# Optimization experiments

Hardware: AMD Instinct MI355X
Metric: run time of the kernel (lower is better)

## Reference

```python
import jax, jax.numpy as jnp
import numpy as np

B, C, N = 4, 256, 4096
OUT = 256
TEMP = OUT ** 0.5  # temperature = sqrt(out_channel)


def setup_inputs() -> dict:
    key = jax.random.key(0)
    kx, kxx, kq, kk, kv = jax.random.split(key, 5)
    x = jax.random.normal(kx, (B, C, N), dtype=jnp.float32)
    xx = jax.random.normal(kxx, (B, C, N), dtype=jnp.float32)
    # Conv1d(in, out, kernel=1, bias=False) weights, squeezed to (out, in)
    s = 1.0 / np.sqrt(C)
    Wq = jax.random.uniform(kq, (OUT, C), jnp.float32, -s, s)
    Wk = jax.random.uniform(kk, (OUT, C), jnp.float32, -s, s)
    Wv = jax.random.uniform(kv, (OUT, C), jnp.float32, -s, s)
    return {"x": x, "xx": xx, "Wq": Wq, "Wk": Wk, "Wv": Wv}


def reference(x, xx, Wq, Wk, Wv):
    # 1x1 conv == per-point linear: (out,in) x (b,in,n) -> (b,out,n)
    q = jnp.einsum('oc,bcn->bon', Wq, x)
    k = jnp.einsum('oc,bcn->bon', Wk, xx)
    v = jnp.einsum('oc,bcn->bon', Wv, xx)
    # attn = (q^T / temp) @ k : (B, N, N)
    attn = jax.nn.softmax(jnp.einsum('bon,bom->bnm', q, k) / TEMP, axis=-1)
    # dropout is identity in eval mode
    # y = attn @ v^T -> (B, N, OUT); returned transposed to (B, OUT, N)
    y = jnp.einsum('bnm,bom->bon', attn, v)
    return y
```

## Files before the change

kernel.cpp:

```cpp
#include <hip/hip_runtime.h>
#include <hip/hip_bf16.h>


typedef __attribute__((ext_vector_type(8))) short bf16x8;
typedef __attribute__((ext_vector_type(4))) float f32x4;
typedef __attribute__((ext_vector_type(4))) short short4t;

constexpr int B_ = 4;
constexpr int C_ = 256;
constexpr int N_ = 4096;
constexpr int O_ = 256;
constexpr float INV_TEMP = 1.0f / 16.0f;
constexpr int NIT = 64;

__device__ __forceinline__ short f2bf(float f) {
  union { float f; unsigned u; } v; v.f = f;
  unsigned r = v.u + 0x7fffu + ((v.u >> 16) & 1u);
  return (short)(r >> 16);
}

__global__ void wcvt(const float* __restrict__ Wq, const float* __restrict__ Wk,
                     const float* __restrict__ Wv, short* __restrict__ wb) {
  int i = blockIdx.x * 256 + threadIdx.x;
  int mat = i >> 16, off = i & 65535;
  const float* W = (mat == 0) ? Wq : (mat == 1 ? Wk : Wv);
  wb[i] = f2bf(W[off]);
}

__global__ __launch_bounds__(256, 2) void qkv_proj(
    const float* __restrict__ x, const float* __restrict__ xx,
    const short* __restrict__ wb,
    short* __restrict__ qg, short* __restrict__ kt, short* __restrict__ vt) {
  const int n0  = blockIdx.x * 64;
  const int b   = blockIdx.y;
  const int mat = blockIdx.z;
  const float* src = (mat == 0) ? x : xx;
  const short* W   = wb + mat * 65536;
  const int tid = threadIdx.x;
  const int w = tid >> 6, lane = tid & 63;
  const int g = lane >> 4, c16 = lane & 15;

  __shared__ __align__(16) short xs[64][264];

  {
    const int n = tid & 63, cq = tid >> 6;
    const float* sp = src + (size_t)b * C_ * N_ + n0 + n;
    float xr[64];
#pragma unroll
    for (int rep = 0; rep < 16; ++rep)
#pragma unroll
      for (int j = 0; j < 4; ++j)
        xr[rep * 4 + j] = sp[(size_t)(rep * 16 + cq * 4 + j) * N_];
#pragma unroll
    for (int rep = 0; rep < 16; ++rep) {
      int c = rep * 16 + cq * 4;
      short4t s4;
#pragma unroll
      for (int j = 0; j < 4; ++j) s4[j] = f2bf(xr[rep * 4 + j]);
      *(short4t*)&xs[n][c] = s4;
    }
  }
  __syncthreads();

  f32x4 acc[4][4];
#pragma unroll
  for (int i = 0; i < 4; ++i)
#pragma unroll
    for (int j = 0; j < 4; ++j) acc[i][j] = (f32x4){0.f, 0.f, 0.f, 0.f};

#pragma unroll
  for (int ko = 0; ko < 8; ++ko) {
    bf16x8 wfr[4], xfr[4];
#pragma unroll
    for (int ot = 0; ot < 4; ++ot)
      wfr[ot] = *(const bf16x8*)&W[(w * 64 + ot * 16 + c16) * C_ + ko * 32 + g * 8];
#pragma unroll
    for (int nt = 0; nt < 4; ++nt)
      xfr[nt] = *(const bf16x8*)&xs[nt * 16 + c16][ko * 32 + g * 8];
    if (mat < 2) {
#pragma unroll
      for (int ot = 0; ot < 4; ++ot)
#pragma unroll
        for (int nt = 0; nt < 4; ++nt)
          acc[ot][nt] = __builtin_amdgcn_mfma_f32_16x16x32_bf16(
              wfr[ot], xfr[nt], acc[ot][nt], 0, 0, 0);
    } else {
#pragma unroll
      for (int mt = 0; mt < 4; ++mt)
#pragma unroll
        for (int ot = 0; ot < 4; ++ot)
          acc[mt][ot] = __builtin_amdgcn_mfma_f32_16x16x32_bf16(
              xfr[mt], wfr[ot], acc[mt][ot], 0, 0, 0);
    }
  }

  __syncthreads();
  short* ob = &xs[0][0];

  if (mat == 0) {
#pragma unroll
    for (int ot = 0; ot < 4; ++ot)
#pragma unroll
      for (int nt = 0; nt < 4; ++nt) {
        int f = (nt * 16 + c16) * 256 + w * 64 + ot * 16 + g * 4;
        short4t s;
        s[0] = f2bf(acc[ot][nt][0] * INV_TEMP);
        s[1] = f2bf(acc[ot][nt][1] * INV_TEMP);
        s[2] = f2bf(acc[ot][nt][2] * INV_TEMP);
        s[3] = f2bf(acc[ot][nt][3] * INV_TEMP);
        *(short4t*)&ob[f] = s;
      }
  } else if (mat == 1) {
#pragma unroll
    for (int ot = 0; ot < 4; ++ot)
#pragma unroll
      for (int nt = 0; nt < 4; ++nt) {
        int koo = w * 2 + (ot >> 1);
        int pos = (((ot & 1) * 2 + (g >> 1)) ^ ((c16 >> 1) & 3));
        int f = nt * 4096 + koo * 512 + c16 * 32 + pos * 8 + (g & 1) * 4;
        short4t s;
        s[0] = f2bf(acc[ot][nt][0]);
        s[1] = f2bf(acc[ot][nt][1]);
        s[2] = f2bf(acc[ot][nt][2]);
        s[3] = f2bf(acc[ot][nt][3]);
        *(short4t*)&ob[f] = s;
      }
  } else {
#pragma unroll
    for (int mt = 0; mt < 4; ++mt)
#pragma unroll
      for (int ot = 0; ot < 4; ++ot) {
        int o = w * 64 + ot * 16 + c16;
        int pos = (mt * 2 + (g >> 1)) ^ (o & 7);
        int f = o * 64 + pos * 8 + (g & 1) * 4;
        short4t s;
        s[0] = f2bf(acc[mt][ot][0]);
        s[1] = f2bf(acc[mt][ot][1]);
        s[2] = f2bf(acc[mt][ot][2]);
        s[3] = f2bf(acc[mt][ot][3]);
        *(short4t*)&ob[f] = s;
      }
  }
  __syncthreads();

  short* dst = (mat == 0) ? qg + ((size_t)b * N_ + n0) * O_
             : (mat == 1) ? kt + (size_t)(b * 256 + (n0 >> 4)) * 4096
                          : vt + (size_t)(b * 64 + (n0 >> 6)) * 16384;
  const uint4* s4 = (const uint4*)ob;
  uint4* d4 = (uint4*)dst;
#pragma unroll
  for (int j = 0; j < 8; ++j) d4[j * 256 + tid] = s4[j * 256 + tid];
}

__global__ __launch_bounds__(512, 4) void flash_attn(
    const short* __restrict__ qg, const short* __restrict__ kt,
    const short* __restrict__ vt, float* __restrict__ out) {
  const int xg = blockIdx.x;
  const int b  = xg & 3;
  const int n0 = (((xg >> 2) << 5) + blockIdx.y) * 32;
  const int tid = threadIdx.x;
  const int w = tid >> 6, lane = tid & 63;
  const int g = lane >> 4, c16 = lane & 15;
  const int pw = w & 3;

  __shared__ short ps[2][32][72];
  __shared__ float lsum[4][32];

  const short* ktb = kt + (size_t)b * N_ * O_;
  const short* vtb = vt + (size_t)b * N_ * O_;

  if (w < 4) {
    bf16x8 qf[2][8];
    bf16x8 kf[8];
    float lrun[2] = {0.f, 0.f};
    const int koff = c16 * 32 + ((g ^ ((c16 >> 1) & 3)) * 8);

#pragma unroll
    for (int nt = 0; nt < 2; ++nt) {
      const short* qrow =
          qg + (size_t)(b * N_ + n0 + nt * 16 + c16) * O_ + g * 8;
#pragma unroll
      for (int ko = 0; ko < 8; ++ko)
        qf[nt][ko] = *(const bf16x8*)(qrow + ko * 32);
    }
    {
      const short* kg = ktb + (size_t)pw * 4096;
#pragma unroll
      for (int j = 0; j < 8; ++j)
        kf[j] = *(const bf16x8*)(kg + j * 512 + koff);
    }

    for (int i = 0; i <= NIT; ++i) {
      if (i < NIT) {
        f32x4 sacc[2];
#pragma unroll
        for (int nt = 0; nt < 2; ++nt) sacc[nt] = (f32x4){0.f, 0.f, 0.f, 0.f};
        __builtin_amdgcn_s_setprio(1);
#pragma unroll
        for (int ko = 0; ko < 8; ++ko) {
#pragma unroll
          for (int nt = 0; nt < 2; ++nt)
            sacc[nt] = __builtin_amdgcn_mfma_f32_16x16x32_bf16(
                kf[ko], qf[nt][ko], sacc[nt], 0, 0, 0);
        }
        __builtin_amdgcn_s_setprio(0);
        if (i + 1 < NIT) {
          const short* kg = ktb + (size_t)(4 * (i + 1) + pw) * 4096;
#pragma unroll
          for (int j = 0; j < 8; ++j)
            kf[j] = *(const bf16x8*)(kg + j * 512 + koff);
        }
#pragma unroll
        for (int nt = 0; nt < 2; ++nt) {
          short4t pb;
          float rs = 0.f;
#pragma unroll
          for (int r = 0; r < 4; ++r) {
            float p = __expf(sacc[nt][r]);
            rs += p;
            pb[r] = f2bf(p);
          }
          lrun[nt] += rs;
          *(short4t*)&ps[i & 1][nt * 16 + c16][pw * 16 + g * 4] = pb;
        }
      }
      asm volatile("s_waitcnt lgkmcnt(0)" ::: "memory");
      __builtin_amdgcn_s_barrier();
    }
#pragma unroll
    for (int nt = 0; nt < 2; ++nt) {
      float v = lrun[nt];
      v += __shfl_xor(v, 16);
      v += __shfl_xor(v, 32);
      if (lane < 16) lsum[pw][nt * 16 + lane] = v;
    }
    asm volatile("s_waitcnt lgkmcnt(0)" ::: "memory");
    __builtin_amdgcn_s_barrier();
  } else {
    bf16x8 vf[8];
    f32x4 oacc[4][2];
#pragma unroll
    for (int i = 0; i < 4; ++i)
#pragma unroll
      for (int j = 0; j < 2; ++j) oacc[i][j] = (f32x4){0.f, 0.f, 0.f, 0.f};

    for (int i = 0; i <= NIT; ++i) {
      if (i > 0) {
        const int pb_ = (i - 1) & 1;
        __builtin_amdgcn_s_setprio(1);
#pragma unroll
        for (int kk = 0; kk < 2; ++kk) {
          bf16x8 pf[2];
#pragma unroll
          for (int nt = 0; nt < 2; ++nt)
            pf[nt] = *(const bf16x8*)&ps[pb_][nt * 16 + c16][kk * 32 + g * 8];
#pragma unroll
          for (int ot = 0; ot < 4; ++ot) {
#pragma unroll
            for (int nt = 0; nt < 2; ++nt)
              oacc[ot][nt] = __builtin_amdgcn_mfma_f32_16x16x32_bf16(
                  vf[kk * 4 + ot], pf[nt], oacc[ot][nt], 0, 0, 0);
          }
        }
        __builtin_amdgcn_s_setprio(0);
      }
      if (i < NIT) {
        const short* vg = vtb + (size_t)i * 16384;
#pragma unroll
        for (int kk = 0; kk < 2; ++kk)
#pragma unroll
          for (int ot = 0; ot < 4; ++ot)
            vf[kk * 4 + ot] = *(const bf16x8*)(
                vg + (pw * 64 + ot * 16 + c16) * 64 +
                ((kk * 4 + g) ^ (c16 & 7)) * 8);
      }
      asm volatile("s_waitcnt lgkmcnt(0)" ::: "memory");
      __builtin_amdgcn_s_barrier();
    }
    __builtin_amdgcn_s_barrier();

#pragma unroll
    for (int nt = 0; nt < 2; ++nt) {
      const int nl = nt * 16 + c16;
      float l = lsum[0][nl] + lsum[1][nl] + lsum[2][nl] + lsum[3][nl];
      float li = 1.0f / l;
#pragma unroll
      for (int ot = 0; ot < 4; ++ot) {
        float* op = out + ((size_t)b * O_ + pw * 64 + ot * 16 + g * 4) * N_ +
                    n0 + nl;
#pragma unroll
        for (int r = 0; r < 4; ++r)
          op[(size_t)r * N_] = oacc[ot][nt][r] * li;
      }
    }
  }
}

extern "C" void kernel_launch(void* const* d_in, const int* in_sizes, int n_in,
                              void* d_out, int out_size, void* d_ws,
                              size_t ws_size, hipStream_t stream) {
  const float* x  = (const float*)d_in[0];
  const float* xx = (const float*)d_in[1];
  const float* Wq = (const float*)d_in[2];
  const float* Wk = (const float*)d_in[3];
  const float* Wv = (const float*)d_in[4];
  float* out = (float*)d_out;

  short* qg = (short*)d_ws;
  short* kt = qg + (size_t)B_ * N_ * O_;
  short* vt = kt + (size_t)B_ * N_ * O_;
  short* wb = vt + (size_t)B_ * N_ * O_;

  wcvt<<<768, 256, 0, stream>>>(Wq, Wk, Wv, wb);
  qkv_proj<<<dim3(N_ / 64, B_, 3), 256, 0, stream>>>(x, xx, wb, qg, kt, vt);
  flash_attn<<<dim3(16, 32), 512, 0, stream>>>(qg, kt, vt, out);
}
```

Baseline: 187.0 us.

## Widen QKV projection tiles to 128 points with 512 threads and vectorized loads

The projection kernel now handles 128 points per block with 8 waves split into 4 output groups by 2 point halves. This halves the grid and reuses each weight fragment load across twice as many points. The input load is changed from scalar strided loads to float4 loads along N, which are then transposed into shared memory, to improve global load coalescing. Shared memory per block doubles (about 67KB), so fewer blocks can be resident on each CU. Only the projection stage changes; the attention kernel, which dominates total time, is untouched.

```diff
diff --git a/kernel.cpp b/kernel.cpp
--- a/kernel.cpp
+++ b/kernel.cpp
@@ -27,11 +27,11 @@
   wb[i] = f2bf(W[off]);
 }
 
-__global__ __launch_bounds__(256, 2) void qkv_proj(
+__global__ __launch_bounds__(512, 4) void qkv_proj(
     const float* __restrict__ x, const float* __restrict__ xx,
     const short* __restrict__ wb,
     short* __restrict__ qg, short* __restrict__ kt, short* __restrict__ vt) {
-  const int n0  = blockIdx.x * 64;
+  const int n0  = blockIdx.x * 128;
   const int b   = blockIdx.y;
   const int mat = blockIdx.z;
   const float* src = (mat == 0) ? x : xx;
@@ -39,25 +39,27 @@
   const int tid = threadIdx.x;
   const int w = tid >> 6, lane = tid & 63;
   const int g = lane >> 4, c16 = lane & 15;
-
-  __shared__ __align__(16) short xs[64][264];
+  const int wo = w & 3, wn = w >> 2;
+
+  __shared__ __align__(16) short xs[128][264];
 
   {
-    const int n = tid & 63, cq = tid >> 6;
-    const float* sp = src + (size_t)b * C_ * N_ + n0 + n;
-    float xr[64];
-#pragma unroll
-    for (int rep = 0; rep < 16; ++rep)
+    const int l5 = lane >> 5, l31 = lane & 31;
+    const float* sp = src + (size_t)b * C_ * N_ + n0 + l31 * 4;
+#pragma unroll
+    for (int q = 0; q < 4; ++q) {
+      const int cb = w * 32 + q * 8 + l5 * 4;
+      f32x4 v[4];
 #pragma unroll
       for (int j = 0; j < 4; ++j)
-        xr[rep * 4 + j] = sp[(size_t)(rep * 16 + cq * 4 + j) * N_];
-#pragma unroll
-    for (int rep = 0; rep < 16; ++rep) {
-      int c = rep * 16 + cq * 4;
-      short4t s4;
-#pragma unroll
-      for (int j = 0; j < 4; ++j) s4[j] = f2bf(xr[rep * 4 + j]);
-      *(short4t*)&xs[n][c] = s4;
+        v[j] = *(const f32x4*)(sp + (size_t)(cb + j) * N_);
+#pragma unroll
+      for (int jj = 0; jj < 4; ++jj) {
+        short4t s4;
+#pragma unroll
+        for (int j = 0; j < 4; ++j) s4[j] = f2bf(v[j][jj]);
+        *(short4t*)&xs[l31 * 4 + jj][cb] = s4;
+      }
     }
   }
   __syncthreads();
@@ -73,10 +75,10 @@
     bf16x8 wfr[4], xfr[4];
 #pragma unroll
     for (int ot = 0; ot < 4; ++ot)
-      wfr[ot] = *(const bf16x8*)&W[(w * 64 + ot * 16 + c16) * C_ + ko * 32 + g * 8];
+      wfr[ot] = *(const bf16x8*)&W[(wo * 64 + ot * 16 + c16) * C_ + ko * 32 + g * 8];
 #pragma unroll
     for (int nt = 0; nt < 4; ++nt)
-      xfr[nt] = *(const bf16x8*)&xs[nt * 16 + c16][ko * 32 + g * 8];
+      xfr[nt] = *(const bf16x8*)&xs[wn * 64 + nt * 16 + c16][ko * 32 + g * 8];
     if (mat < 2) {
 #pragma unroll
       for (int ot = 0; ot < 4; ++ot)
@@ -102,7 +104,7 @@
     for (int ot = 0; ot < 4; ++ot)
 #pragma unroll
       for (int nt = 0; nt < 4; ++nt) {
-        int f = (nt * 16 + c16) * 256 + w * 64 + ot * 16 + g * 4;
+        int f = (wn * 64 + nt * 16 + c16) * 256 + wo * 64 + ot * 16 + g * 4;
         short4t s;
         s[0] = f2bf(acc[ot][nt][0] * INV_TEMP);
         s[1] = f2bf(acc[ot][nt][1] * INV_TEMP);
@@ -115,9 +117,10 @@
     for (int ot = 0; ot < 4; ++ot)
 #pragma unroll
       for (int nt = 0; nt < 4; ++nt) {
-        int koo = w * 2 + (ot >> 1);
+        int gran = wn * 4 + nt;
+        int koo = wo * 2 + (ot >> 1);
         int pos = (((ot & 1) * 2 + (g >> 1)) ^ ((c16 >> 1) & 3));
-        int f = nt * 4096 + koo * 512 + c16 * 32 + pos * 8 + (g & 1) * 4;
+        int f = gran * 4096 + koo * 512 + c16 * 32 + pos * 8 + (g & 1) * 4;
         short4t s;
         s[0] = f2bf(acc[ot][nt][0]);
         s[1] = f2bf(acc[ot][nt][1]);
@@ -130,9 +133,9 @@
     for (int mt = 0; mt < 4; ++mt)
 #pragma unroll
       for (int ot = 0; ot < 4; ++ot) {
-        int o = w * 64 + ot * 16 + c16;
+        int o = wo * 64 + ot * 16 + c16;
         int pos = (mt * 2 + (g >> 1)) ^ (o & 7);
-        int f = o * 64 + pos * 8 + (g & 1) * 4;
+        int f = wn * 16384 + o * 64 + pos * 8 + (g & 1) * 4;
         short4t s;
         s[0] = f2bf(acc[mt][ot][0]);
         s[1] = f2bf(acc[mt][ot][1]);
@@ -146,10 +149,10 @@
   short* dst = (mat == 0) ? qg + ((size_t)b * N_ + n0) * O_
              : (mat == 1) ? kt + (size_t)(b * 256 + (n0 >> 4)) * 4096
                           : vt + (size_t)(b * 64 + (n0 >> 6)) * 16384;
-  const uint4* s4 = (const uint4*)ob;
+  const uint4* s4p = (const uint4*)ob;
   uint4* d4 = (uint4*)dst;
 #pragma unroll
-  for (int j = 0; j < 8; ++j) d4[j * 256 + tid] = s4[j * 256 + tid];
+  for (int j = 0; j < 8; ++j) d4[j * 512 + tid] = s4p[j * 512 + tid];
 }
 
 __global__ __launch_bounds__(512, 4) void flash_attn(
@@ -312,6 +315,6 @@
   short* wb = vt + (size_t)B_ * N_ * O_;
 
   wcvt<<<768, 256, 0, stream>>>(Wq, Wk, Wv, wb);
-  qkv_proj<<<dim3(N_ / 64, B_, 3), 256, 0, stream>>>(x, xx, wb, qg, kt, vt);
+  qkv_proj<<<dim3(N_ / 128, B_, 3), 512, 0, stream>>>(x, xx, wb, qg, kt, vt);
   flash_attn<<<dim3(16, 32), 512, 0, stream>>>(qg, kt, vt, out);
 }
```

Result: slower. 237.3 us (+26.9%).
